# Kernel tuning notes

Measured on AMD Instinct MI355X. Metric: run time of the kernel, lower is better.

## Reference

```python
import jax, jax.numpy as jnp
import numpy as np

T_HORIZON, S_DIM, A_DIM, H = 65536, 128, 8, 256
GAMMA, LMBDA, EPS_CLIP, VF_COEF, ENT_COEF = 0.99, 0.95, 0.2, 0.5, 0.01
LOG2PI = float(np.log(2.0 * np.pi))


def setup_inputs() -> dict:
    key = jax.random.key(0)
    ks = jax.random.split(key, 24)
    s = jax.random.normal(ks[0], (T_HORIZON, S_DIM), jnp.float32)
    a = jax.random.normal(ks[1], (T_HORIZON, A_DIM), jnp.float32)
    r = jax.random.normal(ks[2], (T_HORIZON, 1), jnp.float32)
    sp = jax.random.normal(ks[3], (T_HORIZON, S_DIM), jnp.float32)
    log_prob_a_old = jax.random.normal(ks[4], (T_HORIZON, 1), jnp.float32)
    d_mask = (jax.random.uniform(ks[5], (T_HORIZON, 1)) > 0.05).astype(jnp.float32)

    def lin(k, fan_in, fan_out, std):
        return jax.random.normal(k, (fan_in, fan_out), jnp.float32) * (std / np.sqrt(fan_in))

    params = dict(
        pi_W1=lin(ks[6], S_DIM, H, np.sqrt(2)), pi_b1=jnp.zeros((H,), jnp.float32),
        pi_W2=lin(ks[7], H, H, np.sqrt(2)),     pi_b2=jnp.zeros((H,), jnp.float32),
        mu_W=lin(ks[8], H, A_DIM, 0.01),        mu_b=jnp.zeros((A_DIM,), jnp.float32),
        log_std=jnp.zeros((A_DIM,), jnp.float32),
        v_W1=lin(ks[9], S_DIM, H, np.sqrt(2)),  v_b1=jnp.zeros((H,), jnp.float32),
        v_W2=lin(ks[10], H, H, np.sqrt(2)),     v_b2=jnp.zeros((H,), jnp.float32),
        vh_W=lin(ks[11], H, 1, 1.0),            vh_b=jnp.zeros((1,), jnp.float32),
    )
    return dict(s=s, a=a, r=r, sp=sp, log_prob_a_old=log_prob_a_old, d_mask=d_mask, **params)


def reference(s, a, r, sp, log_prob_a_old, d_mask,
              pi_W1, pi_b1, pi_W2, pi_b2, mu_W, mu_b, log_std,
              v_W1, v_b1, v_W2, v_b2, vh_W, vh_b):
    def mlp(x, W1, b1, W2, b2):
        return jnp.tanh(jnp.tanh(x @ W1 + b1) @ W2 + b2)

    def v_fn(x):
        return mlp(x, v_W1, v_b1, v_W2, v_b2) @ vh_W + vh_b  # [N, 1]

    # ---- GAE (computed under no_grad in the original) ----
    values = jax.lax.stop_gradient(v_fn(s))                  # [T, 1]
    v_last = jax.lax.stop_gradient(v_fn(sp[-1:]))            # [1, 1]
    next_values = jnp.concatenate([values[1:], v_last], axis=0)
    deltas = r + GAMMA * next_values * d_mask - values       # [T, 1]

    def gae_step(gae, inp):
        delta, m = inp
        gae = delta + GAMMA * LMBDA * m * gae
        return gae, gae

    _, advantages = jax.lax.scan(gae_step, jnp.zeros((1,), deltas.dtype),
                                 (deltas, d_mask), reverse=True)  # [T, 1]
    returns = advantages + values
    advantages = (advantages - advantages.mean()) / (advantages.std(ddof=1) + 1e-8)
    advantages = jax.lax.stop_gradient(advantages)
    returns = jax.lax.stop_gradient(returns)

    # ---- PPO clipped loss (single full-batch pass) ----
    mu = mlp(s, pi_W1, pi_b1, pi_W2, pi_b2) @ mu_W + mu_b    # [T, A]
    std = jnp.exp(log_std)
    log_prob = (-0.5 * ((a - mu) / std) ** 2 - log_std - 0.5 * LOG2PI).sum(-1, keepdims=True)
    ratio = jnp.exp(log_prob - log_prob_a_old)               # [T, 1]
    pg_loss = -jnp.minimum(ratio * advantages,
                           jnp.clip(ratio, 1.0 - EPS_CLIP, 1.0 + EPS_CLIP) * advantages).mean()
    diff = v_fn(s) - returns
    vf_loss = jnp.where(jnp.abs(diff) < 1.0, 0.5 * diff ** 2, jnp.abs(diff) - 0.5).mean()
    entropy = (0.5 + 0.5 * LOG2PI + log_std).mean()          # Normal entropy, constant over batch
    return pg_loss + VF_COEF * vf_loss - ENT_COEF * entropy
```

## Files before the change

kernel.cpp:

```cpp
#include <hip/hip_runtime.h>
#include <math.h>

#define TH 65536
#define SD 128
#define AD 8
#define HD 256

constexpr float GAMMA  = 0.99f;
constexpr float LMBDA  = 0.95f;
constexpr float EPSC   = 0.2f;
constexpr float VFC    = 0.5f;
constexpr float ENTC   = 0.01f;
constexpr float LOG2PI = 1.8378770664093453f;

typedef _Float16 half8 __attribute__((ext_vector_type(8)));
typedef __fp16 fp16x2 __attribute__((ext_vector_type(2)));
typedef __attribute__((ext_vector_type(4))) float f32x4;

constexpr size_t WS_VALUES = 0;
constexpr size_t WS_RATIO  = 131080;
constexpr size_t WS_CHP    = 196616;
constexpr size_t WS_CHB    = 196680;
constexpr size_t WS_SCAL   = 196744;
constexpr size_t WS_BF     = 196752;
constexpr size_t SW_PIW1 = 0;
constexpr size_t SW_PIW2 = 32768;
constexpr size_t SW_VW1  = 98304;
constexpr size_t SW_VW2  = 131072;

__device__ __forceinline__ unsigned pk2h(float a, float b) {
    fp16x2 h = __builtin_amdgcn_cvt_pkrtz(a, b);
    return __builtin_bit_cast(unsigned, h);
}

__device__ __forceinline__ float ftanh(float x) {
    float cx = fminf(fmaxf(x, -9.f), 9.f);
    float e = __expf(cx + cx);
    return (e - 1.f) * __builtin_amdgcn_rcpf(e + 1.f);
}

__global__ __launch_bounds__(256) void swizzle_kernel(
    const float* __restrict__ piW1, const float* __restrict__ vW1,
    const float* __restrict__ piW2, const float* __restrict__ vW2,
    unsigned short* __restrict__ dPiW1, unsigned short* __restrict__ dVW1,
    unsigned short* __restrict__ dPiW2, unsigned short* __restrict__ dVW2,
    float* __restrict__ scal)
{
    if (blockIdx.x == 0 && threadIdx.x < 8) scal[threadIdx.x] = 0.f;
    int g = blockIdx.x * 256 + threadIdx.x;
    const float* S; unsigned short* D; int lo;
    if      (g <  8192) { S = piW1; D = dPiW1; lo = 0;     }
    else if (g < 24576) { S = piW2; D = dPiW2; lo = 8192;  }
    else if (g < 32768) { S = vW1;  D = dVW1;  lo = 24576; }
    else                { S = vW2;  D = dVW2;  lo = 32768; }
    int q = g - lo;
    int k = q >> 6, n4 = (q & 63) * 4;
    float4 v = *(const float4*)(S + (size_t)k * HD + n4);
    int ks = k >> 5, kq = (k >> 3) & 3, j = k & 7;
    int nt = n4 >> 4, nr = n4 & 15;
    unsigned short* base = D + ((size_t)(ks * 16 + nt) * 64 + kq * 16 + nr) * 8 + j;
    unsigned p01 = pk2h(v.x, v.y);
    unsigned p23 = pk2h(v.z, v.w);
    base[0]  = (unsigned short)(p01 & 0xffff);
    base[8]  = (unsigned short)(p01 >> 16);
    base[16] = (unsigned short)(p23 & 0xffff);
    base[24] = (unsigned short)(p23 >> 16);
}

__device__ __forceinline__ void runlayer1(
    f32x4* acc, const unsigned short* __restrict__ Ws,
    const half8* afr, int colhalf, int lane)
{
#pragma unroll
    for (int nt = 0; nt < 8; ++nt) acc[nt] = (f32x4){0.f, 0.f, 0.f, 0.f};
#pragma unroll
    for (int ks = 0; ks < 4; ++ks) {
#pragma unroll
        for (int ntl = 0; ntl < 8; ++ntl) {
            half8 bf = ((const half8*)Ws)[(ks * 16 + colhalf * 8 + ntl) * 64 + lane];
            acc[ntl] = __builtin_amdgcn_mfma_f32_16x16x32_f16(afr[ks], bf, acc[ntl], 0, 0, 0);
        }
    }
}

__device__ __forceinline__ void runlayer2(
    f32x4* acc, const unsigned short* __restrict__ Ws,
    const unsigned short* h1, int l15, int quad, int rowgrp, int colhalf, int lane)
{
#pragma unroll
    for (int nt = 0; nt < 8; ++nt) acc[nt] = (f32x4){0.f, 0.f, 0.f, 0.f};
#pragma unroll
    for (int ks = 0; ks < 8; ++ks) {
        half8 af = *(const half8*)(h1 + (rowgrp * 16 + l15) * 264 + ks * 32 + quad * 8);
#pragma unroll
        for (int ntl = 0; ntl < 8; ++ntl) {
            half8 bf = ((const half8*)Ws)[(ks * 16 + colhalf * 8 + ntl) * 64 + lane];
            acc[ntl] = __builtin_amdgcn_mfma_f32_16x16x32_f16(af, bf, acc[ntl], 0, 0, 0);
        }
    }
}

__device__ __forceinline__ void store4(unsigned short* dst, int stride,
                                       float t0, float t1, float t2, float t3)
{
    unsigned p01 = pk2h(t0, t1), p23 = pk2h(t2, t3);
    dst[0]          = (unsigned short)(p01 & 0xffff);
    dst[stride]     = (unsigned short)(p01 >> 16);
    dst[2 * stride] = (unsigned short)(p23 & 0xffff);
    dst[3 * stride] = (unsigned short)(p23 >> 16);
}

__global__ __launch_bounds__(256, 4) void mlp_fused_kernel(
    const float* __restrict__ X, const float* __restrict__ Xlast,
    const unsigned short* __restrict__ piW1s, const float* __restrict__ pib1,
    const unsigned short* __restrict__ piW2s, const float* __restrict__ pib2,
    const float* __restrict__ muW, const float* __restrict__ mub,
    const float* __restrict__ logstd,
    const float* __restrict__ act, const float* __restrict__ lpold,
    const unsigned short* __restrict__ vW1s, const float* __restrict__ vb1,
    const unsigned short* __restrict__ vW2s, const float* __restrict__ vb2,
    const float* __restrict__ vhW, const float* __restrict__ vhb,
    float* __restrict__ values, float* __restrict__ ratio)
{
    __shared__ unsigned short h1[32 * 264];
    __shared__ float cmb[32 * 8];
    __shared__ float val[32];
    const int tid = threadIdx.x;
    const int lane = tid & 63, wave = tid >> 6;
    const int l15 = lane & 15, quad = lane >> 4;
    const int rowgrp = wave >> 1, colhalf = wave & 1;
    const bool vonly = (blockIdx.x == gridDim.x - 1);
    const float* Xp = vonly ? Xlast : X + (size_t)blockIdx.x * 32 * SD;
    const int nrows = vonly ? 1 : 32;
    const int vout0 = vonly ? TH : blockIdx.x * 32;

    if (tid < 32) val[tid] = 0.f;
    cmb[tid] = 0.f;

    const int rr = rowgrp * 16 + l15;
    const float* xrow = Xp + (size_t)(rr < nrows ? rr : 0) * SD;
    half8 afr[4];
#pragma unroll
    for (int ks = 0; ks < 4; ++ks) {
        float4 v0 = *(const float4*)(xrow + ks * 32 + quad * 8);
        float4 v1 = *(const float4*)(xrow + ks * 32 + quad * 8 + 4);
        if (rr >= nrows) { v0 = make_float4(0.f, 0.f, 0.f, 0.f); v1 = v0; }
        uint4 u = make_uint4(pk2h(v0.x, v0.y), pk2h(v0.z, v0.w),
                             pk2h(v1.x, v1.y), pk2h(v1.z, v1.w));
        afr[ks] = __builtin_bit_cast(half8, u);
    }

    f32x4 acc[8];

    if (!vonly) {
        runlayer1(acc, piW1s, afr, colhalf, lane);
#pragma unroll
        for (int ntl = 0; ntl < 8; ++ntl) {
            int col = (colhalf * 8 + ntl) * 16 + l15;
            float bb = pib1[col];
            store4(&h1[(rowgrp * 16 + quad * 4) * 264 + col], 264,
                   ftanh(acc[ntl][0] + bb), ftanh(acc[ntl][1] + bb),
                   ftanh(acc[ntl][2] + bb), ftanh(acc[ntl][3] + bb));
        }
        __syncthreads();
        runlayer2(acc, piW2s, h1, l15, quad, rowgrp, colhalf, lane);
        float pm[4][8];
#pragma unroll
        for (int rg = 0; rg < 4; ++rg)
#pragma unroll
            for (int aj = 0; aj < 8; ++aj) pm[rg][aj] = 0.f;
#pragma unroll
        for (int ntl = 0; ntl < 8; ++ntl) {
            int col = (colhalf * 8 + ntl) * 16 + l15;
            float bb = pib2[col];
            float4 w0 = *(const float4*)(muW + (size_t)col * AD);
            float4 w1 = *(const float4*)(muW + (size_t)col * AD + 4);
            float wv[8] = {w0.x, w0.y, w0.z, w0.w, w1.x, w1.y, w1.z, w1.w};
#pragma unroll
            for (int rg = 0; rg < 4; ++rg) {
                float hv = ftanh(acc[ntl][rg] + bb);
#pragma unroll
                for (int aj = 0; aj < 8; ++aj) pm[rg][aj] = fmaf(hv, wv[aj], pm[rg][aj]);
            }
        }
#pragma unroll
        for (int off = 8; off >= 1; off >>= 1)
#pragma unroll
            for (int rg = 0; rg < 4; ++rg)
#pragma unroll
                for (int aj = 0; aj < 8; ++aj)
                    pm[rg][aj] += __shfl_xor(pm[rg][aj], off, 16);
        if (l15 == 0) {
#pragma unroll
            for (int rg = 0; rg < 4; ++rg) {
                int rowi = rowgrp * 16 + quad * 4 + rg;
#pragma unroll
                for (int aj = 0; aj < 8; ++aj)
                    atomicAdd(&cmb[rowi * 8 + aj], pm[rg][aj]);
            }
        }
        __syncthreads();
        if (tid < 32) {
            int row = blockIdx.x * 32 + tid;
            const float* ar = act + (size_t)row * AD;
            float lp = 0.f;
#pragma unroll
            for (int aj = 0; aj < 8; ++aj) {
                float ls = logstd[aj];
                float mu = cmb[tid * 8 + aj] + mub[aj];
                float z = (ar[aj] - mu) * __expf(-ls);
                lp += -0.5f * z * z - ls;
            }
            lp -= 4.f * LOG2PI;
            ratio[row] = __expf(lp - lpold[row]);
        }
        __syncthreads();
    }

    runlayer1(acc, vW1s, afr, colhalf, lane);
#pragma unroll
    for (int ntl = 0; ntl < 8; ++ntl) {
        int col = (colhalf * 8 + ntl) * 16 + l15;
        float bb = vb1[col];
        store4(&h1[(rowgrp * 16 + quad * 4) * 264 + col], 264,
               ftanh(acc[ntl][0] + bb), ftanh(acc[ntl][1] + bb),
               ftanh(acc[ntl][2] + bb), ftanh(acc[ntl][3] + bb));
    }
    __syncthreads();
    runlayer2(acc, vW2s, h1, l15, quad, rowgrp, colhalf, lane);
    float vp[4] = {0.f, 0.f, 0.f, 0.f};
#pragma unroll
    for (int ntl = 0; ntl < 8; ++ntl) {
        int col = (colhalf * 8 + ntl) * 16 + l15;
        float bb = vb2[col], w = vhW[col];
#pragma unroll
        for (int rg = 0; rg < 4; ++rg) vp[rg] += ftanh(acc[ntl][rg] + bb) * w;
    }
#pragma unroll
    for (int off = 8; off >= 1; off >>= 1)
#pragma unroll
        for (int rg = 0; rg < 4; ++rg) vp[rg] += __shfl_xor(vp[rg], off, 16);
    if (l15 == 0) {
#pragma unroll
        for (int rg = 0; rg < 4; ++rg)
            atomicAdd(&val[rowgrp * 16 + quad * 4 + rg], vp[rg]);
    }
    __syncthreads();
    if (tid < nrows)
        values[vout0 + tid] = val[tid] + vhb[0];
}

__global__ __launch_bounds__(256) void gae_fused_kernel(
    const float* __restrict__ rw, const float* __restrict__ m,
    const float* __restrict__ values, const float* __restrict__ ratio,
    const float* __restrict__ logstd,
    float* __restrict__ chunkP, float* __restrict__ chunkB,
    float* __restrict__ scal, float* __restrict__ out)
{
    __shared__ float sp_[256], sb_[256];
    __shared__ float cp[64], cb[64];
    __shared__ float red[12];
    __shared__ float bcast[4];
    const int j = threadIdx.x;
    const int t0 = blockIdx.x * 1024 + j * 4;
    const float g = GAMMA * LMBDA;

    float4 vv = *(const float4*)(values + t0);
    float v4 = values[t0 + 4];
    float4 rr = *(const float4*)(rw + t0);
    float4 mm = *(const float4*)(m + t0);
    float vs[5] = {vv.x, vv.y, vv.z, vv.w, v4};
    float rs[4] = {rr.x, rr.y, rr.z, rr.w};
    float ms[4] = {mm.x, mm.y, mm.z, mm.w};
    float ds[4];
#pragma unroll
    for (int i = 0; i < 4; ++i)
        ds[i] = rs[i] + GAMMA * vs[i + 1] * ms[i] - vs[i];

    float P = 1.f, B = 0.f;
#pragma unroll
    for (int i = 3; i >= 0; --i) {
        float p = g * ms[i];
        B = ds[i] + p * B;
        P = p * P;
    }
    sp_[j] = P; sb_[j] = B;
    __syncthreads();
    for (int dstep = 1; dstep < 256; dstep <<= 1) {
        float pj = sp_[j], bj = sb_[j], pk = 1.f, bk = 0.f;
        if (j + dstep < 256) { pk = sp_[j + dstep]; bk = sb_[j + dstep]; }
        __syncthreads();
        sp_[j] = pj * pk;
        sb_[j] = bj + pj * bk;
        __syncthreads();
    }
    if (j == 0) {
        atomicExch(&chunkP[blockIdx.x], sp_[0]);
        atomicExch(&chunkB[blockIdx.x], sb_[0]);
        __threadfence();
        atomicAdd(&scal[5], 1.f);
        while (atomicAdd(&scal[5], 0.f) < 64.f) __builtin_amdgcn_s_sleep(2);
    }
    __syncthreads();
    if (j < 64) {
        cp[j] = atomicAdd(&chunkP[j], 0.f);
        cb[j] = atomicAdd(&chunkB[j], 0.f);
    }
    __syncthreads();
    if (j == 0) {
        float A = 0.f;
        for (int c = 63; c > (int)blockIdx.x; --c) A = cb[c] + cp[c] * A;
        bcast[0] = A;
    }
    __syncthreads();
    const float carry = bcast[0];

    float Pe = 1.f, Be = 0.f;
    if (j < 255) { Pe = sp_[j + 1]; Be = sb_[j + 1]; }
    float A = Be + Pe * carry;
    float s1 = 0.f, s2 = 0.f, vf = 0.f;
    float a4[4];
#pragma unroll
    for (int i = 3; i >= 0; --i) {
        A = ds[i] + g * ms[i] * A;
        a4[i] = A;
        float ab = fabsf(A);
        vf += (ab < 1.f) ? 0.5f * A * A : ab - 0.5f;
        s1 += A;
        s2 += A * A;
    }
#pragma unroll
    for (int off = 32; off >= 1; off >>= 1) {
        s1 += __shfl_down(s1, off, 64);
        s2 += __shfl_down(s2, off, 64);
        vf += __shfl_down(vf, off, 64);
    }
    if ((j & 63) == 0) {
        int w = j >> 6;
        red[w] = s1; red[4 + w] = s2; red[8 + w] = vf;
    }
    __syncthreads();
    if (j == 0) {
        atomicAdd(&scal[0], red[0] + red[1] + red[2] + red[3]);
        atomicAdd(&scal[1], red[4] + red[5] + red[6] + red[7]);
        atomicAdd(&scal[2], red[8] + red[9] + red[10] + red[11]);
        __threadfence();
        atomicAdd(&scal[6], 1.f);
        while (atomicAdd(&scal[6], 0.f) < 64.f) __builtin_amdgcn_s_sleep(2);
        bcast[1] = atomicAdd(&scal[0], 0.f);
        bcast[2] = atomicAdd(&scal[1], 0.f);
    }
    __syncthreads();

    const float ssum = bcast[1], ssq = bcast[2];
    const float meanA = ssum / (float)TH;
    const float varA = fmaxf((ssq - ssum * ssum / (float)TH) / (float)(TH - 1), 0.f);
    const float inv = 1.f / (sqrtf(varA) + 1e-8f);

    float4 r4 = *(const float4*)(ratio + t0);
    float rt[4] = {r4.x, r4.y, r4.z, r4.w};
    float pg = 0.f;
#pragma unroll
    for (int i = 0; i < 4; ++i) {
        float aN = (a4[i] - meanA) * inv;
        float rc = fminf(fmaxf(rt[i], 1.f - EPSC), 1.f + EPSC);
        pg -= fminf(rt[i] * aN, rc * aN);
    }
#pragma unroll
    for (int off = 32; off >= 1; off >>= 1) pg += __shfl_down(pg, off, 64);
    if ((j & 63) == 0) red[j >> 6] = pg;
    __syncthreads();
    if (j == 0) {
        atomicAdd(&scal[3], red[0] + red[1] + red[2] + red[3]);
        __threadfence();
        float old = atomicAdd(&scal[4], 1.f);
        if (old == 63.f) {
            float pgs = atomicAdd(&scal[3], 0.f);
            float vfs = atomicAdd(&scal[2], 0.f);
            float ls = 0.f;
#pragma unroll
            for (int jj = 0; jj < AD; ++jj) ls += logstd[jj];
            float entropy = 0.5f + 0.5f * LOG2PI + ls / (float)AD;
            out[0] = pgs / (float)TH + VFC * (vfs / (float)TH) - ENTC * entropy;
        }
    }
}

extern "C" void kernel_launch(void* const* d_in, const int* in_sizes, int n_in,
                              void* d_out, int out_size, void* d_ws, size_t ws_size,
                              hipStream_t stream) {
    const float* s      = (const float*)d_in[0];
    const float* a      = (const float*)d_in[1];
    const float* r      = (const float*)d_in[2];
    const float* sp     = (const float*)d_in[3];
    const float* lpold  = (const float*)d_in[4];
    const float* dmask  = (const float*)d_in[5];
    const float* piW1   = (const float*)d_in[6];
    const float* pib1   = (const float*)d_in[7];
    const float* piW2   = (const float*)d_in[8];
    const float* pib2   = (const float*)d_in[9];
    const float* muW    = (const float*)d_in[10];
    const float* mub    = (const float*)d_in[11];
    const float* logstd = (const float*)d_in[12];
    const float* vW1    = (const float*)d_in[13];
    const float* vb1    = (const float*)d_in[14];
    const float* vW2    = (const float*)d_in[15];
    const float* vb2    = (const float*)d_in[16];
    const float* vhW    = (const float*)d_in[17];
    const float* vhb    = (const float*)d_in[18];

    float* ws      = (float*)d_ws;
    float* values  = ws + WS_VALUES;
    float* ratio   = ws + WS_RATIO;
    float* chunkP  = ws + WS_CHP;
    float* chunkB  = ws + WS_CHB;
    float* scal    = ws + WS_SCAL;
    unsigned short* bfbase = (unsigned short*)(ws + WS_BF);
    unsigned short* dPiW1 = bfbase + SW_PIW1;
    unsigned short* dPiW2 = bfbase + SW_PIW2;
    unsigned short* dVW1  = bfbase + SW_VW1;
    unsigned short* dVW2  = bfbase + SW_VW2;

    swizzle_kernel<<<192, 256, 0, stream>>>(piW1, vW1, piW2, vW2,
                                            dPiW1, dVW1, dPiW2, dVW2, scal);

    mlp_fused_kernel<<<TH / 32 + 1, 256, 0, stream>>>(
        s, sp + (size_t)(TH - 1) * SD,
        dPiW1, pib1, dPiW2, pib2, muW, mub, logstd, a, lpold,
        dVW1, vb1, dVW2, vb2, vhW, vhb,
        values, ratio);

    gae_fused_kernel<<<64, 256, 0, stream>>>(r, dmask, values, ratio, logstd,
                                             chunkP, chunkB, scal, (float*)d_out);
}
```

Measured before the change: 211.0 us.

## Double-buffer MFMA weight loads, simplify tanh, use atomic loads in spin barriers

```diff
diff --git a/kernel.cpp b/kernel.cpp
--- a/kernel.cpp
+++ b/kernel.cpp
@@ -34,9 +34,12 @@
 }
 
 __device__ __forceinline__ float ftanh(float x) {
-    float cx = fminf(fmaxf(x, -9.f), 9.f);
-    float e = __expf(cx + cx);
-    return (e - 1.f) * __builtin_amdgcn_rcpf(e + 1.f);
+    float e = __expf(x + x);
+    return fmaf(-2.f, __builtin_amdgcn_rcpf(e + 1.f), 1.f);
+}
+
+__device__ __forceinline__ float atomLoad(const float* p) {
+    return __hip_atomic_load(p, __ATOMIC_RELAXED, __HIP_MEMORY_SCOPE_AGENT);
 }
 
 __global__ __launch_bounds__(256) void swizzle_kernel(
@@ -71,14 +74,23 @@
     f32x4* acc, const unsigned short* __restrict__ Ws,
     const half8* afr, int colhalf, int lane)
 {
+    const half8* Wp = (const half8*)Ws + (size_t)(colhalf * 8) * 64 + lane;
+    half8 b[2][8];
 #pragma unroll
     for (int nt = 0; nt < 8; ++nt) acc[nt] = (f32x4){0.f, 0.f, 0.f, 0.f};
 #pragma unroll
+    for (int nt = 0; nt < 8; ++nt) b[0][nt] = Wp[(0 * 16 + nt) * 64];
+#pragma unroll
+    for (int nt = 0; nt < 8; ++nt) b[1][nt] = Wp[(1 * 16 + nt) * 64];
+#pragma unroll
     for (int ks = 0; ks < 4; ++ks) {
-#pragma unroll
-        for (int ntl = 0; ntl < 8; ++ntl) {
-            half8 bf = ((const half8*)Ws)[(ks * 16 + colhalf * 8 + ntl) * 64 + lane];
-            acc[ntl] = __builtin_amdgcn_mfma_f32_16x16x32_f16(afr[ks], bf, acc[ntl], 0, 0, 0);
+        const int cur = ks & 1;
+#pragma unroll
+        for (int nt = 0; nt < 8; ++nt)
+            acc[nt] = __builtin_amdgcn_mfma_f32_16x16x32_f16(afr[ks], b[cur][nt], acc[nt], 0, 0, 0);
+        if (ks < 2) {
+#pragma unroll
+            for (int nt = 0; nt < 8; ++nt) b[cur][nt] = Wp[((ks + 2) * 16 + nt) * 64];
         }
     }
 }
@@ -87,15 +99,28 @@
     f32x4* acc, const unsigned short* __restrict__ Ws,
     const unsigned short* h1, int l15, int quad, int rowgrp, int colhalf, int lane)
 {
+    const half8* Wp = (const half8*)Ws + (size_t)(colhalf * 8) * 64 + lane;
+    const unsigned short* Ap = h1 + (rowgrp * 16 + l15) * 264 + quad * 8;
+    half8 b[2][8];
+    half8 af[2];
 #pragma unroll
     for (int nt = 0; nt < 8; ++nt) acc[nt] = (f32x4){0.f, 0.f, 0.f, 0.f};
+    af[0] = *(const half8*)(Ap + 0 * 32);
+#pragma unroll
+    for (int nt = 0; nt < 8; ++nt) b[0][nt] = Wp[(0 * 16 + nt) * 64];
+    af[1] = *(const half8*)(Ap + 1 * 32);
+#pragma unroll
+    for (int nt = 0; nt < 8; ++nt) b[1][nt] = Wp[(1 * 16 + nt) * 64];
 #pragma unroll
     for (int ks = 0; ks < 8; ++ks) {
-        half8 af = *(const half8*)(h1 + (rowgrp * 16 + l15) * 264 + ks * 32 + quad * 8);
-#pragma unroll
-        for (int ntl = 0; ntl < 8; ++ntl) {
-            half8 bf = ((const half8*)Ws)[(ks * 16 + colhalf * 8 + ntl) * 64 + lane];
-            acc[ntl] = __builtin_amdgcn_mfma_f32_16x16x32_f16(af, bf, acc[ntl], 0, 0, 0);
+        const int cur = ks & 1;
+#pragma unroll
+        for (int nt = 0; nt < 8; ++nt)
+            acc[nt] = __builtin_amdgcn_mfma_f32_16x16x32_f16(af[cur], b[cur][nt], acc[nt], 0, 0, 0);
+        if (ks < 6) {
+            af[cur] = *(const half8*)(Ap + (ks + 2) * 32);
+#pragma unroll
+            for (int nt = 0; nt < 8; ++nt) b[cur][nt] = Wp[((ks + 2) * 16 + nt) * 64];
         }
     }
 }
@@ -110,7 +135,7 @@
     dst[3 * stride] = (unsigned short)(p23 >> 16);
 }
 
-__global__ __launch_bounds__(256, 4) void mlp_fused_kernel(
+__global__ __launch_bounds__(256, 3) void mlp_fused_kernel(
     const float* __restrict__ X, const float* __restrict__ Xlast,
     const unsigned short* __restrict__ piW1s, const float* __restrict__ pib1,
     const unsigned short* __restrict__ piW2s, const float* __restrict__ pib2,
@@ -299,12 +324,13 @@
         atomicExch(&chunkB[blockIdx.x], sb_[0]);
         __threadfence();
         atomicAdd(&scal[5], 1.f);
-        while (atomicAdd(&scal[5], 0.f) < 64.f) __builtin_amdgcn_s_sleep(2);
+        while (atomLoad(&scal[5]) < 64.f) __builtin_amdgcn_s_sleep(8);
+        __threadfence();
     }
     __syncthreads();
     if (j < 64) {
-        cp[j] = atomicAdd(&chunkP[j], 0.f);
-        cb[j] = atomicAdd(&chunkB[j], 0.f);
+        cp[j] = atomLoad(&chunkP[j]);
+        cb[j] = atomLoad(&chunkB[j]);
     }
     __syncthreads();
     if (j == 0) {
@@ -346,9 +372,10 @@
         atomicAdd(&scal[2], red[8] + red[9] + red[10] + red[11]);
         __threadfence();
         atomicAdd(&scal[6], 1.f);
-        while (atomicAdd(&scal[6], 0.f) < 64.f) __builtin_amdgcn_s_sleep(2);
-        bcast[1] = atomicAdd(&scal[0], 0.f);
-        bcast[2] = atomicAdd(&scal[1], 0.f);
+        while (atomLoad(&scal[6]) < 64.f) __builtin_amdgcn_s_sleep(8);
+        __threadfence();
+        bcast[1] = atomLoad(&scal[0]);
+        bcast[2] = atomLoad(&scal[1]);
     }
     __syncthreads();
 
@@ -375,8 +402,8 @@
         __threadfence();
         float old = atomicAdd(&scal[4], 1.f);
         if (old == 63.f) {
-            float pgs = atomicAdd(&scal[3], 0.f);
-            float vfs = atomicAdd(&scal[2], 0.f);
+            float pgs = atomLoad(&scal[3]);
+            float vfs = atomLoad(&scal[2]);
             float ls = 0.f;
 #pragma unroll
             for (int jj = 0; jj < AD; ++jj) ls += logstd[jj];
```

After: 216.9 us. 1.03x slower.
